# Performance work log

Measured on AMD Instinct MI355X. Metric: run time of the kernel, lower is better.

Reference implementation:

```python
import jax, jax.numpy as jnp
import numpy as np

ALPHA = 0.2        # LeakyReLU slope
THRESH = 0.01      # sparsity threshold


def setup_inputs() -> dict:
    key = jax.random.key(0)
    ks = jax.random.split(key, 5)
    B, T, F = 32, 128, 32          # batch, seq_len, input_size
    H, HD = 4, 16                  # heads, head_output_size (output_size=64)
    K = 2                          # Chebyshev order
    rank = min(16, F // 2)         # = 16
    x = jax.random.normal(ks[0], (B, T, F), jnp.float32)
    weight = jax.random.normal(ks[1], (K, H, F, HD), jnp.float32) * (1.0 / np.sqrt(F))
    bias = jnp.zeros((H * HD,), jnp.float32)
    temporal_query = jax.random.normal(ks[2], (H, HD), jnp.float32) * 0.1
    temporal_key = jax.random.normal(ks[3], (H, HD), jnp.float32) * 0.1
    feature_factor = jax.random.normal(ks[4], (H, 2, F, rank), jnp.float32) * 0.1
    return dict(x=x, weight=weight, bias=bias, temporal_query=temporal_query,
                temporal_key=temporal_key, feature_factor=feature_factor)


def reference(x, weight, bias, temporal_query, temporal_key, feature_factor):
    # Eval mode (dropout off). k=2: Chebyshev polynomials are [I, L_scaled].
    B, T, F = x.shape
    n = T * F
    x_flat = x.reshape(B, n)
    eye_T = jnp.eye(T, dtype=x.dtype)
    eye_F = jnp.eye(F, dtype=x.dtype)
    eye_n = jnp.eye(n, dtype=x.dtype)
    H = weight.shape[1]
    outs = []
    for h in range(H):
        # --- feature attention (low-rank), softmax over axis 1, threshold ---
        U = feature_factor[h, 0]               # [F, rank]
        V = feature_factor[h, 1]               # [F, rank]
        fa = jax.nn.softmax(jax.nn.leaky_relu(U @ V.T, ALPHA), axis=1)   # [F, F]
        # off-diagonal entries above threshold enter the graph (f1 != f2)
        fa = jnp.where((fa > THRESH) & ~jnp.eye(F, dtype=bool), fa, 0.0)
        # --- temporal attention on x projected by weight[0, h] ---
        xp = x @ weight[0, h]                  # [B, T, HD]
        q = xp @ temporal_query[h][:, None]    # [B, T, 1]
        kk = xp @ temporal_key[h][:, None]     # [B, T, 1]
        tl = jax.nn.leaky_relu(q + jnp.swapaxes(kk, 1, 2), ALPHA).mean(axis=0)  # [T, T]
        ta = jax.nn.softmax(tl, axis=1)
        ta = jnp.where((ta > THRESH) & ~jnp.eye(T, dtype=bool), ta, 0.0)
        # --- sparse graph (Kronecker structure) + self loops ---
        # temporal edges: A[t1*F+f, t2*F+f] = ta[t1,t2] -> kron(ta, I_F)
        # feature edges:  A[t*F+f1, t*F+f2] = fa[f1,f2] -> kron(I_T, fa)
        adj = jnp.kron(ta, eye_F) + jnp.kron(eye_T, fa) + eye_n   # [n, n]
        # --- normalized Laplacian ---
        d_inv_sqrt = (adj.sum(axis=1) + 1e-10) ** -0.5
        L = eye_n - d_inv_sqrt[:, None] * adj * d_inv_sqrt[None, :]
        # --- spectral-norm estimate via 3-step power iteration (no grad) ---
        v = jax.random.normal(jax.random.fold_in(jax.random.key(42), h), (n, 1), x.dtype)
        for _ in range(3):
            v = L @ v
            v = v / (jnp.linalg.norm(v) + 1e-10)
        sn = jnp.maximum(jnp.abs((v.T @ (L @ v))[0, 0]), 1.0)
        sn = jax.lax.stop_gradient(sn)
        L_scaled = 2.0 * L / sn - eye_n
        # --- Chebyshev conv, k=0 filter is identity, k=1 is L_scaled ---
        h0 = x @ weight[0, h]                                    # [B, T, HD]
        h1 = (x_flat @ L_scaled).reshape(B, T, F) @ weight[1, h]  # [B, T, HD]
        outs.append(h0 + h1)
    return jnp.concatenate(outs, axis=2) + bias
```

## Files before the change

### kernel.cpp

```cpp
#include <hip/hip_runtime.h>
#include <cstdint>

static constexpr int Bc = 32, Tc = 128, Fc = 32, Hc = 4, HDc = 16, RKc = 16;
static constexpr int Nc = Tc * Fc;
static constexpr int WS36 = 36;
static constexpr int XLS = 33;

__device__ __forceinline__ uint32_t rotl32(uint32_t v, int r) {
  return (v << r) | (v >> (32 - r));
}

__device__ __forceinline__ void threefry2x32(uint32_t k0, uint32_t k1,
                                             uint32_t& x0, uint32_t& x1) {
  uint32_t k2 = k0 ^ k1 ^ 0x1BD11BDAu;
  x0 += k0; x1 += k1;
#define TF_R(r) { x0 += x1; x1 = rotl32(x1, (r)); x1 ^= x0; }
  TF_R(13) TF_R(15) TF_R(26) TF_R(6)
  x0 += k1; x1 += k2 + 1u;
  TF_R(17) TF_R(29) TF_R(16) TF_R(24)
  x0 += k2; x1 += k0 + 2u;
  TF_R(13) TF_R(15) TF_R(26) TF_R(6)
  x0 += k0; x1 += k1 + 3u;
  TF_R(17) TF_R(29) TF_R(16) TF_R(24)
  x0 += k1; x1 += k2 + 4u;
  TF_R(13) TF_R(15) TF_R(26) TF_R(6)
  x0 += k2; x1 += k0 + 5u;
#undef TF_R
}

__device__ __forceinline__ float erfinv_f32(float x) {
  float w = -__logf((1.0f - x) * (1.0f + x));
  float p;
  if (w < 5.0f) {
    w -= 2.5f;
    p = 2.81022636e-08f;
    p = fmaf(p, w, 3.43273939e-07f);
    p = fmaf(p, w, -3.5233877e-06f);
    p = fmaf(p, w, -4.39150654e-06f);
    p = fmaf(p, w, 0.00021858087f);
    p = fmaf(p, w, -0.00125372503f);
    p = fmaf(p, w, -0.00417768164f);
    p = fmaf(p, w, 0.246640727f);
    p = fmaf(p, w, 1.50140941f);
  } else {
    w = sqrtf(w) - 3.0f;
    p = -0.000200214257f;
    p = fmaf(p, w, 0.000100950558f);
    p = fmaf(p, w, 0.00134934322f);
    p = fmaf(p, w, -0.00367342844f);
    p = fmaf(p, w, 0.00573950773f);
    p = fmaf(p, w, -0.0076224613f);
    p = fmaf(p, w, 0.00943887047f);
    p = fmaf(p, w, 1.00167406f);
    p = fmaf(p, w, 2.83297682f);
  }
  return p * x;
}

__device__ __forceinline__ float jax_normal_from_bits(uint32_t bits) {
  const float lo = -0.99999994f;
  float f = __uint_as_float((bits >> 9) | 0x3f800000u) - 1.0f;
  float u = fmaxf(lo, f * 2.0f + lo);
  return 1.41421354f * erfinv_f32(u);
}

__global__ __launch_bounds__(512)
void proj_kernel(const float* __restrict__ x, const float* __restrict__ weight,
                 const float* __restrict__ tqg, const float* __restrict__ tkg,
                 const float* __restrict__ ffg, float* __restrict__ ws_q,
                 float* __restrict__ ws_k, float* __restrict__ ws_fa,
                 float* __restrict__ ws_rsF) {
  const int b = blockIdx.x;
  const int tid = (int)threadIdx.x;
  __shared__ float xL[Tc * XLS];
  __shared__ float wqS[Hc * Fc], wkS[Hc * Fc];

  const float* xb = x + (size_t)b * Nc;
  for (int j = tid; j < Nc / 4; j += 512) {
    int row = j >> 3, c4 = j & 7;
    float4 v = *(const float4*)&xb[row * Fc + 4 * c4];
    xL[row * XLS + 4 * c4 + 0] = v.x;
    xL[row * XLS + 4 * c4 + 1] = v.y;
    xL[row * XLS + 4 * c4 + 2] = v.z;
    xL[row * XLS + 4 * c4 + 3] = v.w;
  }
  if (tid < Hc * Fc) {
    int h = tid >> 5, f = tid & 31;
    const float* W0 = weight + h * (Fc * HDc) + f * HDc;
    float aq = 0.f, ak = 0.f;
    for (int d = 0; d < HDc; ++d) {
      aq += W0[d] * tqg[h * HDc + d];
      ak += W0[d] * tkg[h * HDc + d];
    }
    wqS[tid] = aq; wkS[tid] = ak;
  }
  if (b < Hc) {
    const int h2 = b;
    for (int j2 = tid; j2 < Fc * Fc; j2 += 512) {
      const float* U = ffg + h2 * (2 * Fc * RKc);
      const float* V = U + Fc * RKc;
      int f1 = j2 >> 5, f2 = j2 & 31;
      float acc = 0.f;
      for (int r = 0; r < RKc; ++r) acc += U[f1 * RKc + r] * V[f2 * RKc + r];
      float val = fmaxf(acc, 0.2f * acc);
      float m = val;
      for (int o = 16; o > 0; o >>= 1) m = fmaxf(m, __shfl_xor(m, o, 32));
      float e = expf(val - m), se = e;
      for (int o = 16; o > 0; o >>= 1) se += __shfl_xor(se, o, 32);
      float pv = e / se;
      pv = (pv > 0.01f && f1 != f2) ? pv : 0.f;
      ws_fa[h2 * (Fc * Fc) + j2] = pv;
      float rsum = pv;
      for (int o = 16; o > 0; o >>= 1) rsum += __shfl_xor(rsum, o, 32);
      if (f2 == 0) ws_rsF[h2 * Fc + f1] = rsum;
    }
  }
  __syncthreads();

  const int t = tid & 127, h = tid >> 7;
  float aq = 0.f, ak = 0.f;
  for (int f = 0; f < Fc; ++f) {
    float xv = xL[t * XLS + f];
    aq += xv * wqS[h * Fc + f];
    ak += xv * wkS[h * Fc + f];
  }
  ws_q[h * Nc + b * Tc + t] = aq;
  ws_k[h * Nc + b * Tc + t] = ak;
}

__global__ __launch_bounds__(256)
void score_kernel(const float* __restrict__ ws_q, const float* __restrict__ ws_k,
                  const float* __restrict__ ws_fa, const float* __restrict__ ws_rsF,
                  float* __restrict__ ws_ta, float* __restrict__ ws_rs,
                  float* __restrict__ ws_pn, float* __restrict__ ws_pd) {
  const int h = blockIdx.x, chunk = blockIdx.y;
  const int tid = (int)threadIdx.x;
  __shared__ float kS[Bc * Tc];
  __shared__ float qS[Bc * 4];
  __shared__ float faTS[Fc * WS36];
  __shared__ float rsFl[Fc];
  __shared__ float rsLoc[4];
  __shared__ float redp[4][2];

  for (int j = tid; j < Bc * Tc / 4; j += 256)
    ((float4*)kS)[j] = ((const float4*)(ws_k + (size_t)h * Nc))[j];
  if (tid < Bc * 4) {
    int b = tid >> 2, r = tid & 3;
    qS[tid] = ws_q[(size_t)h * Nc + b * Tc + 4 * chunk + r];
  }
  for (int i = tid; i < Fc * Fc; i += 256) {
    int f1 = i >> 5, f2 = i & 31;
    faTS[f2 * WS36 + f1] = ws_fa[h * (Fc * Fc) + i];
  }
  if (tid < Fc) rsFl[tid] = ws_rsF[h * Fc + tid];
  __syncthreads();

  const int r = tid >> 6, lane = tid & 63;
  const int gr = 4 * chunk + r;
  float acc0 = 0.f, acc1 = 0.f;
  for (int b = 0; b < Bc; ++b) {
    float q = qS[b * 4 + r];
    float k0 = kS[b * Tc + lane];
    float k1 = kS[b * Tc + lane + 64];
    float s0 = q + k0, s1 = q + k1;
    acc0 += fmaxf(s0, 0.2f * s0);
    acc1 += fmaxf(s1, 0.2f * s1);
  }
  acc0 *= (1.0f / 32.0f);
  acc1 *= (1.0f / 32.0f);
  float m = fmaxf(acc0, acc1);
  for (int o = 32; o > 0; o >>= 1) m = fmaxf(m, __shfl_xor(m, o, 64));
  float e0 = expf(acc0 - m), e1 = expf(acc1 - m);
  float se = e0 + e1;
  for (int o = 32; o > 0; o >>= 1) se += __shfl_xor(se, o, 64);
  float p0 = e0 / se, p1 = e1 / se;
  p0 = ((p0 > 0.01f) && (lane != gr)) ? p0 : 0.f;
  p1 = ((p1 > 0.01f) && (lane + 64 != gr)) ? p1 : 0.f;
  float rs = p0 + p1;
  for (int o = 32; o > 0; o >>= 1) rs += __shfl_xor(rs, o, 64);
  float* tar = ws_ta + (size_t)h * (Tc * Tc) + (size_t)gr * Tc;
  tar[lane] = p0;
  tar[lane + 64] = p1;
  if (lane == 0) { ws_rs[h * Tc + gr] = rs; rsLoc[r] = rs; }
  __syncthreads();

  if (tid < 128) {
    const int g = tid >> 5, f = tid & 31;
    const int t = 4 * chunk + g;
    float s = 1.0f / sqrtf(rsLoc[g] + rsFl[f] + 1.0f + 1e-10f);
    float v;
    {
      uint32_t fk0 = 0u, fk1 = (uint32_t)h;
      threefry2x32(0u, 42u, fk0, fk1);
      int l = t * Fc + f;
      int pr = l & 2047;
      uint32_t c0 = (uint32_t)pr, c1 = (uint32_t)(pr + 2048);
      threefry2x32(fk0, fk1, c0, c1);
      v = jax_normal_from_bits(l < 2048 ? c0 : c1);
    }
    float u4v = 0.f;
    for (int it = 0; it < 4; ++it) {
      float w = s * v;
      float acc = 0.f;
#pragma unroll
      for (int f2 = 0; f2 < Fc; ++f2) {
        float ww = __shfl(w, f2, 32);
        acc += faTS[f2 * WS36 + f] * ww;
      }
      float nv = v - s * (acc + w);
      if (it < 3) v = nv; else u4v = nv;
    }
    float pn = v * u4v, pd = v * v;
    for (int o = 16; o > 0; o >>= 1) {
      pn += __shfl_xor(pn, o, 32);
      pd += __shfl_xor(pd, o, 32);
    }
    if (f == 0) { redp[g][0] = pn; redp[g][1] = pd; }
  }
  __syncthreads();
  if (tid == 0) {
    float num = redp[0][0] + redp[1][0] + redp[2][0] + redp[3][0];
    float den = redp[0][1] + redp[1][1] + redp[2][1] + redp[3][1];
    ws_pn[h * 32 + chunk] = num;
    ws_pd[h * 32 + chunk] = den;
  }
}

__global__ __launch_bounds__(512, 1)
void conv_kernel(const float* __restrict__ x, const float* __restrict__ weight,
                 const float* __restrict__ bias, const float* __restrict__ ws_ta,
                 const float* __restrict__ ws_rs, const float* __restrict__ ws_fa,
                 const float* __restrict__ ws_rsF, const float* __restrict__ ws_pn,
                 const float* __restrict__ ws_pd, float* __restrict__ out) {
  const int b = blockIdx.x, h = blockIdx.y;
  const int tid = (int)threadIdx.x;
  const int lane = tid & 63, wvi = tid >> 6;

  __shared__ __align__(16) float faS[Fc * WS36];
  __shared__ __align__(16) float faTS[Fc * WS36];
  __shared__ __align__(16) float W0s[Fc * HDc];
  __shared__ __align__(16) float W1s[Fc * HDc];
  __shared__ __align__(16) float wbuf[Tc * WS36];
  __shared__ __align__(16) float vtmp[Nc];
  __shared__ float rsT[Tc], rsF[Fc];
  __shared__ float pnL[32], pdL[32];
  __shared__ float red[8][2];
  __shared__ int flagS;

  const int t = tid >> 2, fq = tid & 3, f0 = 8 * fq;

  if (tid < Tc) rsT[tid] = ws_rs[h * Tc + tid];
  if (tid < Fc) rsF[tid] = ws_rsF[h * Fc + tid];
  {
    W0s[tid] = weight[h * (Fc * HDc) + tid];
    W1s[tid] = weight[(Hc + h) * (Fc * HDc) + tid];
  }
  for (int i = tid; i < Fc * Fc; i += 512) {
    float fv = ws_fa[h * (Fc * Fc) + i];
    faS[(i >> 5) * WS36 + (i & 31)] = fv;
    faTS[(i & 31) * WS36 + (i >> 5)] = fv;
  }
  if (tid < 32) { pnL[tid] = ws_pn[h * 32 + tid]; pdL[tid] = ws_pd[h * 32 + tid]; }
  if (tid < 64) {
    int nz = (ws_rs[h * Tc + tid] > 0.f) || (ws_rs[h * Tc + tid + 64] > 0.f);
    unsigned long long bal = __ballot(nz);
    if (tid == 0) flagS = (bal != 0ull) ? 1 : 0;
  }
  const float* xb = x + (size_t)b * Nc;
  float4 xva = *(const float4*)&xb[t * Fc + f0];
  float4 xvb = *(const float4*)&xb[t * Fc + f0 + 4];
  __syncthreads();

  float s_reg[8];
  {
    float rrow = rsT[t];
#pragma unroll
    for (int j = 0; j < 8; ++j)
      s_reg[j] = 1.0f / sqrtf(rrow + rsF[f0 + j] + 1.0f + 1e-10f);
  }

  float sn;
  if (!flagS) {
    float num = 0.f, den = 0.f;
#pragma unroll
    for (int i2 = 0; i2 < 32; ++i2) { num += pnL[i2]; den += pdL[i2]; }
    sn = fmaxf(fabsf(num / den), 1.0f);
  } else {
    {
      uint32_t fk0 = 0u, fk1 = (uint32_t)h;
      threefry2x32(0u, 42u, fk0, fk1);
      float n0[4], n1[4];
#pragma unroll
      for (int jj = 0; jj < 4; ++jj) {
        int l = tid * 4 + jj;
        uint32_t c0 = (uint32_t)l, c1 = (uint32_t)(l + 2048);
        threefry2x32(fk0, fk1, c0, c1);
        n0[jj] = jax_normal_from_bits(c0);
        n1[jj] = jax_normal_from_bits(c1);
      }
      *(float4*)&vtmp[tid * 4]        = make_float4(n0[0], n0[1], n0[2], n0[3]);
      *(float4*)&vtmp[2048 + tid * 4] = make_float4(n1[0], n1[1], n1[2], n1[3]);
    }
    __syncthreads();
    float v[8];
    {
      float4 v0a = *(const float4*)&vtmp[t * Fc + f0];
      float4 v0b = *(const float4*)&vtmp[t * Fc + f0 + 4];
      v[0]=v0a.x; v[1]=v0a.y; v[2]=v0a.z; v[3]=v0a.w;
      v[4]=v0b.x; v[5]=v0b.y; v[6]=v0b.z; v[7]=v0b.w;
    }
    const int srcBase = lane & 60;
    float u4[8];
    for (int it = 0; it < 4; ++it) {
      float w[8];
#pragma unroll
      for (int j = 0; j < 8; ++j) w[j] = s_reg[j] * v[j];
      *(float4*)&wbuf[t * WS36 + f0]     = make_float4(w[0], w[1], w[2], w[3]);
      *(float4*)&wbuf[t * WS36 + f0 + 4] = make_float4(w[4], w[5], w[6], w[7]);
      __syncthreads();
      float wrow[32];
#pragma unroll
      for (int oq = 0; oq < 4; ++oq)
#pragma unroll
        for (int j = 0; j < 8; ++j)
          wrow[oq * 8 + j] = __shfl(w[j], srcBase + oq, 64);
      float acc[8] = {};
#pragma unroll
      for (int f2 = 0; f2 < Fc; ++f2) {
        float4 fa0 = *(const float4*)&faTS[f2 * WS36 + f0];
        float4 fa1 = *(const float4*)&faTS[f2 * WS36 + f0 + 4];
        float ww = wrow[f2];
        acc[0] += ww * fa0.x; acc[1] += ww * fa0.y;
        acc[2] += ww * fa0.z; acc[3] += ww * fa0.w;
        acc[4] += ww * fa1.x; acc[5] += ww * fa1.y;
        acc[6] += ww * fa1.z; acc[7] += ww * fa1.w;
      }
      {
        const float* taG = ws_ta + (size_t)h * (Tc * Tc) + (size_t)t * Tc;
        for (int k = 0; k < Tc; ++k) {
          float tak = taG[k];
          float4 w0 = *(const float4*)&wbuf[k * WS36 + f0];
          float4 w1 = *(const float4*)&wbuf[k * WS36 + f0 + 4];
          acc[0] += tak * w0.x; acc[1] += tak * w0.y;
          acc[2] += tak * w0.z; acc[3] += tak * w0.w;
          acc[4] += tak * w1.x; acc[5] += tak * w1.y;
          acc[6] += tak * w1.z; acc[7] += tak * w1.w;
        }
      }
      __syncthreads();
      float nv[8];
#pragma unroll
      for (int j = 0; j < 8; ++j) {
        float a = acc[j] + w[j];
        nv[j] = v[j] - s_reg[j] * a;
      }
      if (it < 3) {
#pragma unroll
        for (int j = 0; j < 8; ++j) v[j] = nv[j];
      } else {
#pragma unroll
        for (int j = 0; j < 8; ++j) u4[j] = nv[j];
      }
    }
    float pn = 0.f, pd = 0.f;
#pragma unroll
    for (int j = 0; j < 8; ++j) { pn += v[j] * u4[j]; pd += v[j] * v[j]; }
    for (int o = 32; o > 0; o >>= 1) {
      pn += __shfl_down(pn, o, 64);
      pd += __shfl_down(pd, o, 64);
    }
    if (lane == 0) { red[wvi][0] = pn; red[wvi][1] = pd; }
    __syncthreads();
    float num = 0.f, den = 0.f;
#pragma unroll
    for (int i2 = 0; i2 < 8; ++i2) { num += red[i2][0]; den += red[i2][1]; }
    sn = fmaxf(fabsf(num / den), 1.0f);
  }
  const float csn = 2.0f / sn;
  const float cm1 = csn - 1.0f;

  float X[8] = {xva.x, xva.y, xva.z, xva.w, xvb.x, xvb.y, xvb.z, xvb.w};
  float Z[8];
#pragma unroll
  for (int j = 0; j < 8; ++j) Z[j] = s_reg[j] * X[j];

  float gacc[8] = {};
  if (flagS) {
    __syncthreads();
    *(float4*)&wbuf[t * WS36 + f0]     = make_float4(Z[0], Z[1], Z[2], Z[3]);
    *(float4*)&wbuf[t * WS36 + f0 + 4] = make_float4(Z[4], Z[5], Z[6], Z[7]);
    __syncthreads();
    const float* taG = ws_ta + (size_t)h * (Tc * Tc);
    for (int k = 0; k < Tc; ++k) {
      float tak = taG[(size_t)k * Tc + t];
      float4 z0 = *(const float4*)&wbuf[k * WS36 + f0];
      float4 z1 = *(const float4*)&wbuf[k * WS36 + f0 + 4];
      gacc[0] += tak * z0.x; gacc[1] += tak * z0.y;
      gacc[2] += tak * z0.z; gacc[3] += tak * z0.w;
      gacc[4] += tak * z1.x; gacc[5] += tak * z1.y;
      gacc[6] += tak * z1.z; gacc[7] += tak * z1.w;
    }
  }
  {
    const int srcBase = lane & 60;
    float zrow[32];
#pragma unroll
    for (int oq = 0; oq < 4; ++oq)
#pragma unroll
      for (int j = 0; j < 8; ++j)
        zrow[oq * 8 + j] = __shfl(Z[j], srcBase + oq, 64);
#pragma unroll
    for (int f2 = 0; f2 < Fc; ++f2) {
      float4 fa0 = *(const float4*)&faS[f2 * WS36 + f0];
      float4 fa1 = *(const float4*)&faS[f2 * WS36 + f0 + 4];
      float zz = zrow[f2];
      gacc[0] += zz * fa0.x; gacc[1] += zz * fa0.y;
      gacc[2] += zz * fa0.z; gacc[3] += zz * fa0.w;
      gacc[4] += zz * fa1.x; gacc[5] += zz * fa1.y;
      gacc[6] += zz * fa1.z; gacc[7] += zz * fa1.w;
    }
  }
  float G[8];
#pragma unroll
  for (int j = 0; j < 8; ++j)
    G[j] = cm1 * X[j] - csn * s_reg[j] * (gacc[j] + Z[j]);

  float acc2[16] = {};
#pragma unroll
  for (int jf = 0; jf < 8; ++jf) {
    int f = f0 + jf;
#pragma unroll
    for (int hq = 0; hq < 4; ++hq) {
      float4 w0 = *(const float4*)&W0s[f * HDc + 4 * hq];
      float4 w1 = *(const float4*)&W1s[f * HDc + 4 * hq];
      acc2[4*hq+0] += X[jf] * w0.x + G[jf] * w1.x;
      acc2[4*hq+1] += X[jf] * w0.y + G[jf] * w1.y;
      acc2[4*hq+2] += X[jf] * w0.z + G[jf] * w1.z;
      acc2[4*hq+3] += X[jf] * w0.w + G[jf] * w1.w;
    }
  }
#pragma unroll
  for (int i2 = 0; i2 < 16; ++i2) {
    acc2[i2] += __shfl_xor(acc2[i2], 1, 64);
    acc2[i2] += __shfl_xor(acc2[i2], 2, 64);
  }
  {
    float4 bv = *(const float4*)&bias[h * HDc + 4 * fq];
    float4 o4;
    if      (fq == 0) o4 = make_float4(acc2[0],  acc2[1],  acc2[2],  acc2[3]);
    else if (fq == 1) o4 = make_float4(acc2[4],  acc2[5],  acc2[6],  acc2[7]);
    else if (fq == 2) o4 = make_float4(acc2[8],  acc2[9],  acc2[10], acc2[11]);
    else              o4 = make_float4(acc2[12], acc2[13], acc2[14], acc2[15]);
    o4.x += bv.x; o4.y += bv.y; o4.z += bv.z; o4.w += bv.w;
    *(float4*)&out[((size_t)b * Tc + t) * (Hc * HDc) + h * HDc + 4 * fq] = o4;
  }
}

extern "C" void kernel_launch(void* const* d_in, const int* in_sizes, int n_in,
                              void* d_out, int out_size, void* d_ws, size_t ws_size,
                              hipStream_t stream) {
  const float* x      = (const float*)d_in[0];
  const float* weight = (const float*)d_in[1];
  const float* bias   = (const float*)d_in[2];
  const float* tqg    = (const float*)d_in[3];
  const float* tkg    = (const float*)d_in[4];
  const float* ffg    = (const float*)d_in[5];
  float* out = (float*)d_out;

  float* ws = (float*)d_ws;
  float* ws_ta  = ws;
  float* ws_rs  = ws + 65536;
  float* ws_q   = ws + 66048;
  float* ws_k   = ws + 82432;
  float* ws_fa  = ws + 98816;
  float* ws_rsF = ws + 102912;
  float* ws_pn  = ws + 103040;
  float* ws_pd  = ws + 103168;

  proj_kernel<<<dim3(Bc), dim3(512), 0, stream>>>(
      x, weight, tqg, tkg, ffg, ws_q, ws_k, ws_fa, ws_rsF);
  score_kernel<<<dim3(Hc, 32), dim3(256), 0, stream>>>(
      ws_q, ws_k, ws_fa, ws_rsF, ws_ta, ws_rs, ws_pn, ws_pd);
  conv_kernel<<<dim3(Bc, Hc), dim3(512), 0, stream>>>(
      x, weight, bias, ws_ta, ws_rs, ws_fa, ws_rsF, ws_pn, ws_pd, out);
}
```

Baseline: 28.15 us.

## Fuse three kernels into one cooperative kernel with grid-wide syncs

Merges the projection, score and convolution kernels into one cooperative launch of 128 blocks, with grid.sync() separating the phases and a single shared-memory buffer carved differently in each phase. The goal is to remove two kernel launch gaps and their inter-kernel drain and refill on a very short pipeline. In exchange it pays for grid-wide barriers and a cooperative launch, and the projection phase now uses only a few of the blocks.

```diff
diff --git a/kernel.cpp b/kernel.cpp
--- a/kernel.cpp
+++ b/kernel.cpp
@@ -1,5 +1,8 @@
 #include <hip/hip_runtime.h>
+#include <hip/hip_cooperative_groups.h>
 #include <cstdint>
+
+namespace cg = cooperative_groups;
 
 static constexpr int Bc = 32, Tc = 128, Fc = 32, Hc = 4, HDc = 16, RKc = 16;
 static constexpr int Nc = Tc * Fc;
@@ -64,38 +67,61 @@
   return 1.41421354f * erfinv_f32(u);
 }
 
-__global__ __launch_bounds__(512)
-void proj_kernel(const float* __restrict__ x, const float* __restrict__ weight,
-                 const float* __restrict__ tqg, const float* __restrict__ tkg,
-                 const float* __restrict__ ffg, float* __restrict__ ws_q,
-                 float* __restrict__ ws_k, float* __restrict__ ws_fa,
-                 float* __restrict__ ws_rsF) {
-  const int b = blockIdx.x;
+__global__ __launch_bounds__(512, 1)
+void mono_kernel(const float* __restrict__ x, const float* __restrict__ weight,
+                 const float* __restrict__ bias, const float* __restrict__ tqg,
+                 const float* __restrict__ tkg, const float* __restrict__ ffg,
+                 float* __restrict__ ws_q, float* __restrict__ ws_k,
+                 float* __restrict__ ws_fa, float* __restrict__ ws_rsF,
+                 float* __restrict__ ws_ta, float* __restrict__ ws_rs,
+                 float* __restrict__ ws_pn, float* __restrict__ ws_pd,
+                 float* __restrict__ out) {
+  cg::grid_group grid = cg::this_grid();
+  const int bid = (int)blockIdx.x;
   const int tid = (int)threadIdx.x;
-  __shared__ float xL[Tc * XLS];
-  __shared__ float wqS[Hc * Fc], wkS[Hc * Fc];
-
-  const float* xb = x + (size_t)b * Nc;
-  for (int j = tid; j < Nc / 4; j += 512) {
-    int row = j >> 3, c4 = j & 7;
-    float4 v = *(const float4*)&xb[row * Fc + 4 * c4];
-    xL[row * XLS + 4 * c4 + 0] = v.x;
-    xL[row * XLS + 4 * c4 + 1] = v.y;
-    xL[row * XLS + 4 * c4 + 2] = v.z;
-    xL[row * XLS + 4 * c4 + 3] = v.w;
-  }
-  if (tid < Hc * Fc) {
-    int h = tid >> 5, f = tid & 31;
-    const float* W0 = weight + h * (Fc * HDc) + f * HDc;
+  const int lane = tid & 63, wvi = tid >> 6;
+
+  __shared__ __align__(16) float sm[12288];
+  __shared__ int flagS;
+
+  if (bid < Bc) {
+    const int b = bid;
+    float* xL  = sm;
+    float* wqS = sm + 4224;
+    float* wkS = sm + 4352;
+
+    const float* xb = x + (size_t)b * Nc;
+    for (int j = tid; j < Nc / 4; j += 512) {
+      int row = j >> 3, c4 = j & 7;
+      float4 v = *(const float4*)&xb[row * Fc + 4 * c4];
+      xL[row * XLS + 4 * c4 + 0] = v.x;
+      xL[row * XLS + 4 * c4 + 1] = v.y;
+      xL[row * XLS + 4 * c4 + 2] = v.z;
+      xL[row * XLS + 4 * c4 + 3] = v.w;
+    }
+    if (tid < Hc * Fc) {
+      int h = tid >> 5, f = tid & 31;
+      const float* W0 = weight + h * (Fc * HDc) + f * HDc;
+      float aq = 0.f, ak = 0.f;
+      for (int d = 0; d < HDc; ++d) {
+        aq += W0[d] * tqg[h * HDc + d];
+        ak += W0[d] * tkg[h * HDc + d];
+      }
+      wqS[tid] = aq; wkS[tid] = ak;
+    }
+    __syncthreads();
+
+    const int t = tid & 127, h = tid >> 7;
     float aq = 0.f, ak = 0.f;
-    for (int d = 0; d < HDc; ++d) {
-      aq += W0[d] * tqg[h * HDc + d];
-      ak += W0[d] * tkg[h * HDc + d];
-    }
-    wqS[tid] = aq; wkS[tid] = ak;
-  }
-  if (b < Hc) {
-    const int h2 = b;
+    for (int f = 0; f < Fc; ++f) {
+      float xv = xL[t * XLS + f];
+      aq += xv * wqS[h * Fc + f];
+      ak += xv * wkS[h * Fc + f];
+    }
+    ws_q[h * Nc + b * Tc + t] = aq;
+    ws_k[h * Nc + b * Tc + t] = ak;
+  } else if (bid < Bc + Hc) {
+    const int h2 = bid - Bc;
     for (int j2 = tid; j2 < Fc * Fc; j2 += 512) {
       const float* U = ffg + h2 * (2 * Fc * RKc);
       const float* V = U + Fc * RKc;
@@ -115,344 +141,325 @@
       if (f2 == 0) ws_rsF[h2 * Fc + f1] = rsum;
     }
   }
-  __syncthreads();
-
-  const int t = tid & 127, h = tid >> 7;
-  float aq = 0.f, ak = 0.f;
-  for (int f = 0; f < Fc; ++f) {
-    float xv = xL[t * XLS + f];
-    aq += xv * wqS[h * Fc + f];
-    ak += xv * wkS[h * Fc + f];
+  grid.sync();
+
+  {
+    const int h = bid >> 5, chunk = bid & 31;
+    float* kS    = sm;
+    float* qS    = sm + 4096;
+    float* faTS  = sm + 4224;
+    float* rsFl  = sm + 5376;
+    float* rsLoc = sm + 5408;
+    float* redp  = sm + 5416;
+
+    for (int j = tid; j < Bc * Tc / 4; j += 512)
+      ((float4*)kS)[j] = ((const float4*)(ws_k + (size_t)h * Nc))[j];
+    if (tid < Bc * 4) {
+      int b2 = tid >> 2, r = tid & 3;
+      qS[tid] = ws_q[(size_t)h * Nc + b2 * Tc + 4 * chunk + r];
+    }
+    for (int i = tid; i < Fc * Fc; i += 512) {
+      int f1 = i >> 5, f2 = i & 31;
+      faTS[f2 * WS36 + f1] = ws_fa[h * (Fc * Fc) + i];
+    }
+    if (tid < Fc) rsFl[tid] = ws_rsF[h * Fc + tid];
+    __syncthreads();
+
+    if (tid < 256) {
+      const int r = tid >> 6, ln = tid & 63;
+      const int gr = 4 * chunk + r;
+      float acc0 = 0.f, acc1 = 0.f;
+      for (int b2 = 0; b2 < Bc; ++b2) {
+        float q = qS[b2 * 4 + r];
+        float k0 = kS[b2 * Tc + ln];
+        float k1 = kS[b2 * Tc + ln + 64];
+        float s0 = q + k0, s1 = q + k1;
+        acc0 += fmaxf(s0, 0.2f * s0);
+        acc1 += fmaxf(s1, 0.2f * s1);
+      }
+      acc0 *= (1.0f / 32.0f);
+      acc1 *= (1.0f / 32.0f);
+      float m = fmaxf(acc0, acc1);
+      for (int o = 32; o > 0; o >>= 1) m = fmaxf(m, __shfl_xor(m, o, 64));
+      float e0 = expf(acc0 - m), e1 = expf(acc1 - m);
+      float se = e0 + e1;
+      for (int o = 32; o > 0; o >>= 1) se += __shfl_xor(se, o, 64);
+      float p0 = e0 / se, p1 = e1 / se;
+      p0 = ((p0 > 0.01f) && (ln != gr)) ? p0 : 0.f;
+      p1 = ((p1 > 0.01f) && (ln + 64 != gr)) ? p1 : 0.f;
+      float rs = p0 + p1;
+      for (int o = 32; o > 0; o >>= 1) rs += __shfl_xor(rs, o, 64);
+      float* tar = ws_ta + (size_t)h * (Tc * Tc) + (size_t)gr * Tc;
+      tar[ln] = p0;
+      tar[ln + 64] = p1;
+      if (ln == 0) { ws_rs[h * Tc + gr] = rs; rsLoc[r] = rs; }
+    }
+    __syncthreads();
+
+    if (tid < 128) {
+      const int g = tid >> 5, f = tid & 31;
+      const int t = 4 * chunk + g;
+      float s = 1.0f / sqrtf(rsLoc[g] + rsFl[f] + 1.0f + 1e-10f);
+      float v;
+      {
+        uint32_t fk0 = 0u, fk1 = (uint32_t)h;
+        threefry2x32(0u, 42u, fk0, fk1);
+        int l = t * Fc + f;
+        int pr = l & 2047;
+        uint32_t c0 = (uint32_t)pr, c1 = (uint32_t)(pr + 2048);
+        threefry2x32(fk0, fk1, c0, c1);
+        v = jax_normal_from_bits(l < 2048 ? c0 : c1);
+      }
+      float u4v = 0.f;
+      for (int it = 0; it < 4; ++it) {
+        float w = s * v;
+        float acc = 0.f;
+#pragma unroll
+        for (int f2 = 0; f2 < Fc; ++f2) {
+          float ww = __shfl(w, f2, 32);
+          acc += faTS[f2 * WS36 + f] * ww;
+        }
+        float nv = v - s * (acc + w);
+        if (it < 3) v = nv; else u4v = nv;
+      }
+      float pn = v * u4v, pd = v * v;
+      for (int o = 16; o > 0; o >>= 1) {
+        pn += __shfl_xor(pn, o, 32);
+        pd += __shfl_xor(pd, o, 32);
+      }
+      if (f == 0) { redp[2 * g] = pn; redp[2 * g + 1] = pd; }
+    }
+    __syncthreads();
+    if (tid == 0) {
+      float num = redp[0] + redp[2] + redp[4] + redp[6];
+      float den = redp[1] + redp[3] + redp[5] + redp[7];
+      ws_pn[h * 32 + chunk] = num;
+      ws_pd[h * 32 + chunk] = den;
+    }
   }
-  ws_q[h * Nc + b * Tc + t] = aq;
-  ws_k[h * Nc + b * Tc + t] = ak;
-}
-
-__global__ __launch_bounds__(256)
-void score_kernel(const float* __restrict__ ws_q, const float* __restrict__ ws_k,
-                  const float* __restrict__ ws_fa, const float* __restrict__ ws_rsF,
-                  float* __restrict__ ws_ta, float* __restrict__ ws_rs,
-                  float* __restrict__ ws_pn, float* __restrict__ ws_pd) {
-  const int h = blockIdx.x, chunk = blockIdx.y;
-  const int tid = (int)threadIdx.x;
-  __shared__ float kS[Bc * Tc];
-  __shared__ float qS[Bc * 4];
-  __shared__ float faTS[Fc * WS36];
-  __shared__ float rsFl[Fc];
-  __shared__ float rsLoc[4];
-  __shared__ float redp[4][2];
-
-  for (int j = tid; j < Bc * Tc / 4; j += 256)
-    ((float4*)kS)[j] = ((const float4*)(ws_k + (size_t)h * Nc))[j];
-  if (tid < Bc * 4) {
-    int b = tid >> 2, r = tid & 3;
-    qS[tid] = ws_q[(size_t)h * Nc + b * Tc + 4 * chunk + r];
-  }
-  for (int i = tid; i < Fc * Fc; i += 256) {
-    int f1 = i >> 5, f2 = i & 31;
-    faTS[f2 * WS36 + f1] = ws_fa[h * (Fc * Fc) + i];
-  }
-  if (tid < Fc) rsFl[tid] = ws_rsF[h * Fc + tid];
-  __syncthreads();
-
-  const int r = tid >> 6, lane = tid & 63;
-  const int gr = 4 * chunk + r;
-  float acc0 = 0.f, acc1 = 0.f;
-  for (int b = 0; b < Bc; ++b) {
-    float q = qS[b * 4 + r];
-    float k0 = kS[b * Tc + lane];
-    float k1 = kS[b * Tc + lane + 64];
-    float s0 = q + k0, s1 = q + k1;
-    acc0 += fmaxf(s0, 0.2f * s0);
-    acc1 += fmaxf(s1, 0.2f * s1);
-  }
-  acc0 *= (1.0f / 32.0f);
-  acc1 *= (1.0f / 32.0f);
-  float m = fmaxf(acc0, acc1);
-  for (int o = 32; o > 0; o >>= 1) m = fmaxf(m, __shfl_xor(m, o, 64));
-  float e0 = expf(acc0 - m), e1 = expf(acc1 - m);
-  float se = e0 + e1;
-  for (int o = 32; o > 0; o >>= 1) se += __shfl_xor(se, o, 64);
-  float p0 = e0 / se, p1 = e1 / se;
-  p0 = ((p0 > 0.01f) && (lane != gr)) ? p0 : 0.f;
-  p1 = ((p1 > 0.01f) && (lane + 64 != gr)) ? p1 : 0.f;
-  float rs = p0 + p1;
-  for (int o = 32; o > 0; o >>= 1) rs += __shfl_xor(rs, o, 64);
-  float* tar = ws_ta + (size_t)h * (Tc * Tc) + (size_t)gr * Tc;
-  tar[lane] = p0;
-  tar[lane + 64] = p1;
-  if (lane == 0) { ws_rs[h * Tc + gr] = rs; rsLoc[r] = rs; }
-  __syncthreads();
-
-  if (tid < 128) {
-    const int g = tid >> 5, f = tid & 31;
-    const int t = 4 * chunk + g;
-    float s = 1.0f / sqrtf(rsLoc[g] + rsFl[f] + 1.0f + 1e-10f);
-    float v;
+  grid.sync();
+
+  {
+    const int h = bid >> 5, b = bid & 31;
+    float* faS   = sm;
+    float* faTS  = sm + 1152;
+    float* W0s   = sm + 2304;
+    float* W1s   = sm + 2816;
+    float* wbuf  = sm + 3328;
+    float* vtmp  = sm + 7936;
+    float* rsT   = sm + 12032;
+    float* rsF   = sm + 12160;
+    float* pnL   = sm + 12192;
+    float* pdL   = sm + 12224;
+    float* red   = sm + 12256;
+
+    const int t = tid >> 2, fq = tid & 3, f0 = 8 * fq;
+
+    if (tid < Tc) rsT[tid] = ws_rs[h * Tc + tid];
+    if (tid < Fc) rsF[tid] = ws_rsF[h * Fc + tid];
     {
-      uint32_t fk0 = 0u, fk1 = (uint32_t)h;
-      threefry2x32(0u, 42u, fk0, fk1);
-      int l = t * Fc + f;
-      int pr = l & 2047;
-      uint32_t c0 = (uint32_t)pr, c1 = (uint32_t)(pr + 2048);
-      threefry2x32(fk0, fk1, c0, c1);
-      v = jax_normal_from_bits(l < 2048 ? c0 : c1);
-    }
-    float u4v = 0.f;
-    for (int it = 0; it < 4; ++it) {
-      float w = s * v;
-      float acc = 0.f;
+      W0s[tid] = weight[h * (Fc * HDc) + tid];
+      W1s[tid] = weight[(Hc + h) * (Fc * HDc) + tid];
+    }
+    for (int i = tid; i < Fc * Fc; i += 512) {
+      float fv = ws_fa[h * (Fc * Fc) + i];
+      faS[(i >> 5) * WS36 + (i & 31)] = fv;
+      faTS[(i & 31) * WS36 + (i >> 5)] = fv;
+    }
+    if (tid < 32) { pnL[tid] = ws_pn[h * 32 + tid]; pdL[tid] = ws_pd[h * 32 + tid]; }
+    if (tid < 64) {
+      int nz = (ws_rs[h * Tc + tid] > 0.f) || (ws_rs[h * Tc + tid + 64] > 0.f);
+      unsigned long long bal = __ballot(nz);
+      if (tid == 0) flagS = (bal != 0ull) ? 1 : 0;
+    }
+    const float* xb = x + (size_t)b * Nc;
+    float4 xva = *(const float4*)&xb[t * Fc + f0];
+    float4 xvb = *(const float4*)&xb[t * Fc + f0 + 4];
+    __syncthreads();
+
+    float s_reg[8];
+    {
+      float rrow = rsT[t];
+#pragma unroll
+      for (int j = 0; j < 8; ++j)
+        s_reg[j] = 1.0f / sqrtf(rrow + rsF[f0 + j] + 1.0f + 1e-10f);
+    }
+
+    float sn;
+    if (!flagS) {
+      float num = 0.f, den = 0.f;
+#pragma unroll
+      for (int i2 = 0; i2 < 32; ++i2) { num += pnL[i2]; den += pdL[i2]; }
+      sn = fmaxf(fabsf(num / den), 1.0f);
+    } else {
+      {
+        uint32_t fk0 = 0u, fk1 = (uint32_t)h;
+        threefry2x32(0u, 42u, fk0, fk1);
+        float n0[4], n1[4];
+#pragma unroll
+        for (int jj = 0; jj < 4; ++jj) {
+          int l = tid * 4 + jj;
+          uint32_t c0 = (uint32_t)l, c1 = (uint32_t)(l + 2048);
+          threefry2x32(fk0, fk1, c0, c1);
+          n0[jj] = jax_normal_from_bits(c0);
+          n1[jj] = jax_normal_from_bits(c1);
+        }
+        *(float4*)&vtmp[tid * 4]        = make_float4(n0[0], n0[1], n0[2], n0[3]);
+        *(float4*)&vtmp[2048 + tid * 4] = make_float4(n1[0], n1[1], n1[2], n1[3]);
+      }
+      __syncthreads();
+      float v[8];
+      {
+        float4 v0a = *(const float4*)&vtmp[t * Fc + f0];
+        float4 v0b = *(const float4*)&vtmp[t * Fc + f0 + 4];
+        v[0]=v0a.x; v[1]=v0a.y; v[2]=v0a.z; v[3]=v0a.w;
+        v[4]=v0b.x; v[5]=v0b.y; v[6]=v0b.z; v[7]=v0b.w;
+      }
+      const int srcBase = lane & 60;
+      float u4[8];
+      for (int it = 0; it < 4; ++it) {
+        float w[8];
+#pragma unroll
+        for (int j = 0; j < 8; ++j) w[j] = s_reg[j] * v[j];
+        *(float4*)&wbuf[t * WS36 + f0]     = make_float4(w[0], w[1], w[2], w[3]);
+        *(float4*)&wbuf[t * WS36 + f0 + 4] = make_float4(w[4], w[5], w[6], w[7]);
+        __syncthreads();
+        float wrow[32];
+#pragma unroll
+        for (int oq = 0; oq < 4; ++oq)
+#pragma unroll
+          for (int j = 0; j < 8; ++j)
+            wrow[oq * 8 + j] = __shfl(w[j], srcBase + oq, 64);
+        float acc[8] = {};
+#pragma unroll
+        for (int f2 = 0; f2 < Fc; ++f2) {
+          float4 fa0 = *(const float4*)&faTS[f2 * WS36 + f0];
+          float4 fa1 = *(const float4*)&faTS[f2 * WS36 + f0 + 4];
+          float ww = wrow[f2];
+          acc[0] += ww * fa0.x; acc[1] += ww * fa0.y;
+          acc[2] += ww * fa0.z; acc[3] += ww * fa0.w;
+          acc[4] += ww * fa1.x; acc[5] += ww * fa1.y;
+          acc[6] += ww * fa1.z; acc[7] += ww * fa1.w;
+        }
+        {
+          const float* taG = ws_ta + (size_t)h * (Tc * Tc) + (size_t)t * Tc;
+          for (int k = 0; k < Tc; ++k) {
+            float tak = taG[k];
+            float4 w0 = *(const float4*)&wbuf[k * WS36 + f0];
+            float4 w1 = *(const float4*)&wbuf[k * WS36 + f0 + 4];
+            acc[0] += tak * w0.x; acc[1] += tak * w0.y;
+            acc[2] += tak * w0.z; acc[3] += tak * w0.w;
+            acc[4] += tak * w1.x; acc[5] += tak * w1.y;
+            acc[6] += tak * w1.z; acc[7] += tak * w1.w;
+          }
+        }
+        __syncthreads();
+        float nv[8];
+#pragma unroll
+        for (int j = 0; j < 8; ++j) {
+          float a = acc[j] + w[j];
+          nv[j] = v[j] - s_reg[j] * a;
+        }
+        if (it < 3) {
+#pragma unroll
+          for (int j = 0; j < 8; ++j) v[j] = nv[j];
+        } else {
+#pragma unroll
+          for (int j = 0; j < 8; ++j) u4[j] = nv[j];
+        }
+      }
+      float pn = 0.f, pd = 0.f;
+#pragma unroll
+      for (int j = 0; j < 8; ++j) { pn += v[j] * u4[j]; pd += v[j] * v[j]; }
+      for (int o = 32; o > 0; o >>= 1) {
+        pn += __shfl_down(pn, o, 64);
+        pd += __shfl_down(pd, o, 64);
+      }
+      if (lane == 0) { red[2 * wvi] = pn; red[2 * wvi + 1] = pd; }
+      __syncthreads();
+      float num = 0.f, den = 0.f;
+#pragma unroll
+      for (int i2 = 0; i2 < 8; ++i2) { num += red[2 * i2]; den += red[2 * i2 + 1]; }
+      sn = fmaxf(fabsf(num / den), 1.0f);
+    }
+    const float csn = 2.0f / sn;
+    const float cm1 = csn - 1.0f;
+
+    float X[8] = {xva.x, xva.y, xva.z, xva.w, xvb.x, xvb.y, xvb.z, xvb.w};
+    float Z[8];
+#pragma unroll
+    for (int j = 0; j < 8; ++j) Z[j] = s_reg[j] * X[j];
+
+    float gacc[8] = {};
+    if (flagS) {
+      __syncthreads();
+      *(float4*)&wbuf[t * WS36 + f0]     = make_float4(Z[0], Z[1], Z[2], Z[3]);
+      *(float4*)&wbuf[t * WS36 + f0 + 4] = make_float4(Z[4], Z[5], Z[6], Z[7]);
+      __syncthreads();
+      const float* taG = ws_ta + (size_t)h * (Tc * Tc);
+      for (int k = 0; k < Tc; ++k) {
+        float tak = taG[(size_t)k * Tc + t];
+        float4 z0 = *(const float4*)&wbuf[k * WS36 + f0];
+        float4 z1 = *(const float4*)&wbuf[k * WS36 + f0 + 4];
+        gacc[0] += tak * z0.x; gacc[1] += tak * z0.y;
+        gacc[2] += tak * z0.z; gacc[3] += tak * z0.w;
+        gacc[4] += tak * z1.x; gacc[5] += tak * z1.y;
+        gacc[6] += tak * z1.z; gacc[7] += tak * z1.w;
+      }
+    }
+    {
+      const int srcBase = lane & 60;
+      float zrow[32];
+#pragma unroll
+      for (int oq = 0; oq < 4; ++oq)
+#pragma unroll
+        for (int j = 0; j < 8; ++j)
+          zrow[oq * 8 + j] = __shfl(Z[j], srcBase + oq, 64);
 #pragma unroll
       for (int f2 = 0; f2 < Fc; ++f2) {
-        float ww = __shfl(w, f2, 32);
-        acc += faTS[f2 * WS36 + f] * ww;
-      }
-      float nv = v - s * (acc + w);
-      if (it < 3) v = nv; else u4v = nv;
-    }
-    float pn = v * u4v, pd = v * v;
-    for (int o = 16; o > 0; o >>= 1) {
-      pn += __shfl_xor(pn, o, 32);
-      pd += __shfl_xor(pd, o, 32);
-    }
-    if (f == 0) { redp[g][0] = pn; redp[g][1] = pd; }
-  }
-  __syncthreads();
-  if (tid == 0) {
-    float num = redp[0][0] + redp[1][0] + redp[2][0] + redp[3][0];
-    float den = redp[0][1] + redp[1][1] + redp[2][1] + redp[3][1];
-    ws_pn[h * 32 + chunk] = num;
-    ws_pd[h * 32 + chunk] = den;
-  }
-}
-
-__global__ __launch_bounds__(512, 1)
-void conv_kernel(const float* __restrict__ x, const float* __restrict__ weight,
-                 const float* __restrict__ bias, const float* __restrict__ ws_ta,
-                 const float* __restrict__ ws_rs, const float* __restrict__ ws_fa,
-                 const float* __restrict__ ws_rsF, const float* __restrict__ ws_pn,
-                 const float* __restrict__ ws_pd, float* __restrict__ out) {
-  const int b = blockIdx.x, h = blockIdx.y;
-  const int tid = (int)threadIdx.x;
-  const int lane = tid & 63, wvi = tid >> 6;
-
-  __shared__ __align__(16) float faS[Fc * WS36];
-  __shared__ __align__(16) float faTS[Fc * WS36];
-  __shared__ __align__(16) float W0s[Fc * HDc];
-  __shared__ __align__(16) float W1s[Fc * HDc];
-  __shared__ __align__(16) float wbuf[Tc * WS36];
-  __shared__ __align__(16) float vtmp[Nc];
-  __shared__ float rsT[Tc], rsF[Fc];
-  __shared__ float pnL[32], pdL[32];
-  __shared__ float red[8][2];
-  __shared__ int flagS;
-
-  const int t = tid >> 2, fq = tid & 3, f0 = 8 * fq;
-
-  if (tid < Tc) rsT[tid] = ws_rs[h * Tc + tid];
-  if (tid < Fc) rsF[tid] = ws_rsF[h * Fc + tid];
-  {
-    W0s[tid] = weight[h * (Fc * HDc) + tid];
-    W1s[tid] = weight[(Hc + h) * (Fc * HDc) + tid];
-  }
-  for (int i = tid; i < Fc * Fc; i += 512) {
-    float fv = ws_fa[h * (Fc * Fc) + i];
-    faS[(i >> 5) * WS36 + (i & 31)] = fv;
-    faTS[(i & 31) * WS36 + (i >> 5)] = fv;
-  }
-  if (tid < 32) { pnL[tid] = ws_pn[h * 32 + tid]; pdL[tid] = ws_pd[h * 32 + tid]; }
-  if (tid < 64) {
-    int nz = (ws_rs[h * Tc + tid] > 0.f) || (ws_rs[h * Tc + tid + 64] > 0.f);
-    unsigned long long bal = __ballot(nz);
-    if (tid == 0) flagS = (bal != 0ull) ? 1 : 0;
-  }
-  const float* xb = x + (size_t)b * Nc;
-  float4 xva = *(const float4*)&xb[t * Fc + f0];
-  float4 xvb = *(const float4*)&xb[t * Fc + f0 + 4];
-  __syncthreads();
-
-  float s_reg[8];
-  {
-    float rrow = rsT[t];
+        float4 fa0 = *(const float4*)&faS[f2 * WS36 + f0];
+        float4 fa1 = *(const float4*)&faS[f2 * WS36 + f0 + 4];
+        float zz = zrow[f2];
+        gacc[0] += zz * fa0.x; gacc[1] += zz * fa0.y;
+        gacc[2] += zz * fa0.z; gacc[3] += zz * fa0.w;
+        gacc[4] += zz * fa1.x; gacc[5] += zz * fa1.y;
+        gacc[6] += zz * fa1.z; gacc[7] += zz * fa1.w;
+      }
+    }
+    float G[8];
 #pragma unroll
     for (int j = 0; j < 8; ++j)
-      s_reg[j] = 1.0f / sqrtf(rrow + rsF[f0 + j] + 1.0f + 1e-10f);
-  }
-
-  float sn;
-  if (!flagS) {
-    float num = 0.f, den = 0.f;
-#pragma unroll
-    for (int i2 = 0; i2 < 32; ++i2) { num += pnL[i2]; den += pdL[i2]; }
-    sn = fmaxf(fabsf(num / den), 1.0f);
-  } else {
+      G[j] = cm1 * X[j] - csn * s_reg[j] * (gacc[j] + Z[j]);
+
+    float acc2[16] = {};
+#pragma unroll
+    for (int jf = 0; jf < 8; ++jf) {
+      int f = f0 + jf;
+#pragma unroll
+      for (int hq = 0; hq < 4; ++hq) {
+        float4 w0 = *(const float4*)&W0s[f * HDc + 4 * hq];
+        float4 w1 = *(const float4*)&W1s[f * HDc + 4 * hq];
+        acc2[4*hq+0] += X[jf] * w0.x + G[jf] * w1.x;
+        acc2[4*hq+1] += X[jf] * w0.y + G[jf] * w1.y;
+        acc2[4*hq+2] += X[jf] * w0.z + G[jf] * w1.z;
+        acc2[4*hq+3] += X[jf] * w0.w + G[jf] * w1.w;
+      }
+    }
+#pragma unroll
+    for (int i2 = 0; i2 < 16; ++i2) {
+      acc2[i2] += __shfl_xor(acc2[i2], 1, 64);
+      acc2[i2] += __shfl_xor(acc2[i2], 2, 64);
+    }
     {
-      uint32_t fk0 = 0u, fk1 = (uint32_t)h;
-      threefry2x32(0u, 42u, fk0, fk1);
-      float n0[4], n1[4];
-#pragma unroll
-      for (int jj = 0; jj < 4; ++jj) {
-        int l = tid * 4 + jj;
-        uint32_t c0 = (uint32_t)l, c1 = (uint32_t)(l + 2048);
-        threefry2x32(fk0, fk1, c0, c1);
-        n0[jj] = jax_normal_from_bits(c0);
-        n1[jj] = jax_normal_from_bits(c1);
-      }
-      *(float4*)&vtmp[tid * 4]        = make_float4(n0[0], n0[1], n0[2], n0[3]);
-      *(float4*)&vtmp[2048 + tid * 4] = make_float4(n1[0], n1[1], n1[2], n1[3]);
-    }
-    __syncthreads();
-    float v[8];
-    {
-      float4 v0a = *(const float4*)&vtmp[t * Fc + f0];
-      float4 v0b = *(const float4*)&vtmp[t * Fc + f0 + 4];
-      v[0]=v0a.x; v[1]=v0a.y; v[2]=v0a.z; v[3]=v0a.w;
-      v[4]=v0b.x; v[5]=v0b.y; v[6]=v0b.z; v[7]=v0b.w;
-    }
-    const int srcBase = lane & 60;
-    float u4[8];
-    for (int it = 0; it < 4; ++it) {
-      float w[8];
-#pragma unroll
-      for (int j = 0; j < 8; ++j) w[j] = s_reg[j] * v[j];
-      *(float4*)&wbuf[t * WS36 + f0]     = make_float4(w[0], w[1], w[2], w[3]);
-      *(float4*)&wbuf[t * WS36 + f0 + 4] = make_float4(w[4], w[5], w[6], w[7]);
-      __syncthreads();
-      float wrow[32];
-#pragma unroll
-      for (int oq = 0; oq < 4; ++oq)
-#pragma unroll
-        for (int j = 0; j < 8; ++j)
-          wrow[oq * 8 + j] = __shfl(w[j], srcBase + oq, 64);
-      float acc[8] = {};
-#pragma unroll
-      for (int f2 = 0; f2 < Fc; ++f2) {
-        float4 fa0 = *(const float4*)&faTS[f2 * WS36 + f0];
-        float4 fa1 = *(const float4*)&faTS[f2 * WS36 + f0 + 4];
-        float ww = wrow[f2];
-        acc[0] += ww * fa0.x; acc[1] += ww * fa0.y;
-        acc[2] += ww * fa0.z; acc[3] += ww * fa0.w;
-        acc[4] += ww * fa1.x; acc[5] += ww * fa1.y;
-        acc[6] += ww * fa1.z; acc[7] += ww * fa1.w;
-      }
-      {
-        const float* taG = ws_ta + (size_t)h * (Tc * Tc) + (size_t)t * Tc;
-        for (int k = 0; k < Tc; ++k) {
-          float tak = taG[k];
-          float4 w0 = *(const float4*)&wbuf[k * WS36 + f0];
-          float4 w1 = *(const float4*)&wbuf[k * WS36 + f0 + 4];
-          acc[0] += tak * w0.x; acc[1] += tak * w0.y;
-          acc[2] += tak * w0.z; acc[3] += tak * w0.w;
-          acc[4] += tak * w1.x; acc[5] += tak * w1.y;
-          acc[6] += tak * w1.z; acc[7] += tak * w1.w;
-        }
-      }
-      __syncthreads();
-      float nv[8];
-#pragma unroll
-      for (int j = 0; j < 8; ++j) {
-        float a = acc[j] + w[j];
-        nv[j] = v[j] - s_reg[j] * a;
-      }
-      if (it < 3) {
-#pragma unroll
-        for (int j = 0; j < 8; ++j) v[j] = nv[j];
-      } else {
-#pragma unroll
-        for (int j = 0; j < 8; ++j) u4[j] = nv[j];
-      }
-    }
-    float pn = 0.f, pd = 0.f;
-#pragma unroll
-    for (int j = 0; j < 8; ++j) { pn += v[j] * u4[j]; pd += v[j] * v[j]; }
-    for (int o = 32; o > 0; o >>= 1) {
-      pn += __shfl_down(pn, o, 64);
-      pd += __shfl_down(pd, o, 64);
-    }
-    if (lane == 0) { red[wvi][0] = pn; red[wvi][1] = pd; }
-    __syncthreads();
-    float num = 0.f, den = 0.f;
-#pragma unroll
-    for (int i2 = 0; i2 < 8; ++i2) { num += red[i2][0]; den += red[i2][1]; }
-    sn = fmaxf(fabsf(num / den), 1.0f);
-  }
-  const float csn = 2.0f / sn;
-  const float cm1 = csn - 1.0f;
-
-  float X[8] = {xva.x, xva.y, xva.z, xva.w, xvb.x, xvb.y, xvb.z, xvb.w};
-  float Z[8];
-#pragma unroll
-  for (int j = 0; j < 8; ++j) Z[j] = s_reg[j] * X[j];
-
-  float gacc[8] = {};
-  if (flagS) {
-    __syncthreads();
-    *(float4*)&wbuf[t * WS36 + f0]     = make_float4(Z[0], Z[1], Z[2], Z[3]);
-    *(float4*)&wbuf[t * WS36 + f0 + 4] = make_float4(Z[4], Z[5], Z[6], Z[7]);
-    __syncthreads();
-    const float* taG = ws_ta + (size_t)h * (Tc * Tc);
-    for (int k = 0; k < Tc; ++k) {
-      float tak = taG[(size_t)k * Tc + t];
-      float4 z0 = *(const float4*)&wbuf[k * WS36 + f0];
-      float4 z1 = *(const float4*)&wbuf[k * WS36 + f0 + 4];
-      gacc[0] += tak * z0.x; gacc[1] += tak * z0.y;
-      gacc[2] += tak * z0.z; gacc[3] += tak * z0.w;
-      gacc[4] += tak * z1.x; gacc[5] += tak * z1.y;
-      gacc[6] += tak * z1.z; gacc[7] += tak * z1.w;
-    }
-  }
-  {
-    const int srcBase = lane & 60;
-    float zrow[32];
-#pragma unroll
-    for (int oq = 0; oq < 4; ++oq)
-#pragma unroll
-      for (int j = 0; j < 8; ++j)
-        zrow[oq * 8 + j] = __shfl(Z[j], srcBase + oq, 64);
-#pragma unroll
-    for (int f2 = 0; f2 < Fc; ++f2) {
-      float4 fa0 = *(const float4*)&faS[f2 * WS36 + f0];
-      float4 fa1 = *(const float4*)&faS[f2 * WS36 + f0 + 4];
-      float zz = zrow[f2];
-      gacc[0] += zz * fa0.x; gacc[1] += zz * fa0.y;
-      gacc[2] += zz * fa0.z; gacc[3] += zz * fa0.w;
-      gacc[4] += zz * fa1.x; gacc[5] += zz * fa1.y;
-      gacc[6] += zz * fa1.z; gacc[7] += zz * fa1.w;
-    }
-  }
-  float G[8];
-#pragma unroll
-  for (int j = 0; j < 8; ++j)
-    G[j] = cm1 * X[j] - csn * s_reg[j] * (gacc[j] + Z[j]);
-
-  float acc2[16] = {};
-#pragma unroll
-  for (int jf = 0; jf < 8; ++jf) {
-    int f = f0 + jf;
-#pragma unroll
-    for (int hq = 0; hq < 4; ++hq) {
-      float4 w0 = *(const float4*)&W0s[f * HDc + 4 * hq];
-      float4 w1 = *(const float4*)&W1s[f * HDc + 4 * hq];
-      acc2[4*hq+0] += X[jf] * w0.x + G[jf] * w1.x;
-      acc2[4*hq+1] += X[jf] * w0.y + G[jf] * w1.y;
-      acc2[4*hq+2] += X[jf] * w0.z + G[jf] * w1.z;
-      acc2[4*hq+3] += X[jf] * w0.w + G[jf] * w1.w;
-    }
-  }
-#pragma unroll
-  for (int i2 = 0; i2 < 16; ++i2) {
-    acc2[i2] += __shfl_xor(acc2[i2], 1, 64);
-    acc2[i2] += __shfl_xor(acc2[i2], 2, 64);
-  }
-  {
-    float4 bv = *(const float4*)&bias[h * HDc + 4 * fq];
-    float4 o4;
-    if      (fq == 0) o4 = make_float4(acc2[0],  acc2[1],  acc2[2],  acc2[3]);
-    else if (fq == 1) o4 = make_float4(acc2[4],  acc2[5],  acc2[6],  acc2[7]);
-    else if (fq == 2) o4 = make_float4(acc2[8],  acc2[9],  acc2[10], acc2[11]);
-    else              o4 = make_float4(acc2[12], acc2[13], acc2[14], acc2[15]);
-    o4.x += bv.x; o4.y += bv.y; o4.z += bv.z; o4.w += bv.w;
-    *(float4*)&out[((size_t)b * Tc + t) * (Hc * HDc) + h * HDc + 4 * fq] = o4;
+      float4 bv = *(const float4*)&bias[h * HDc + 4 * fq];
+      float4 o4;
+      if      (fq == 0) o4 = make_float4(acc2[0],  acc2[1],  acc2[2],  acc2[3]);
+      else if (fq == 1) o4 = make_float4(acc2[4],  acc2[5],  acc2[6],  acc2[7]);
+      else if (fq == 2) o4 = make_float4(acc2[8],  acc2[9],  acc2[10], acc2[11]);
+      else              o4 = make_float4(acc2[12], acc2[13], acc2[14], acc2[15]);
+      o4.x += bv.x; o4.y += bv.y; o4.z += bv.z; o4.w += bv.w;
+      *(float4*)&out[((size_t)b * Tc + t) * (Hc * HDc) + h * HDc + 4 * fq] = o4;
+    }
   }
 }
 
@@ -477,10 +484,10 @@
   float* ws_pn  = ws + 103040;
   float* ws_pd  = ws + 103168;
 
-  proj_kernel<<<dim3(Bc), dim3(512), 0, stream>>>(
-      x, weight, tqg, tkg, ffg, ws_q, ws_k, ws_fa, ws_rsF);
-  score_kernel<<<dim3(Hc, 32), dim3(256), 0, stream>>>(
-      ws_q, ws_k, ws_fa, ws_rsF, ws_ta, ws_rs, ws_pn, ws_pd);
-  conv_kernel<<<dim3(Bc, Hc), dim3(512), 0, stream>>>(
-      x, weight, bias, ws_ta, ws_rs, ws_fa, ws_rsF, ws_pn, ws_pd, out);
-}
+  void* args[] = {(void*)&x, (void*)&weight, (void*)&bias, (void*)&tqg,
+                  (void*)&tkg, (void*)&ffg, (void*)&ws_q, (void*)&ws_k,
+                  (void*)&ws_fa, (void*)&ws_rsF, (void*)&ws_ta, (void*)&ws_rs,
+                  (void*)&ws_pn, (void*)&ws_pd, (void*)&out};
+  hipLaunchCooperativeKernel((void*)mono_kernel, dim3(128), dim3(512),
+                             args, 0, stream);
+}
```

After: 65.34 us. +132.1%, slower.
